# Kernel optimization log

Measured on AMD Instinct MI355X. Metric: run time of the kernel, lower is better.

Reference implementation:

```python
import jax, jax.numpy as jnp
import numpy as np

B, T, S, C = 4096, 128, 16, 128
NEG = -1e30  # finite stand-in for -inf to keep grads NaN-free


def setup_inputs() -> dict:
    key = jax.random.key(0)
    k1, k2 = jax.random.split(key)
    prediction = jax.random.normal(k1, (B, T, C), dtype=jnp.float32)  # treated as log-probs, as in the original
    lable = jax.random.normal(k2, (B, S, C), dtype=jnp.float32)       # one-hot-ish label scores
    return {"prediction": prediction, "lable": lable}


def _ctc_nll(logp, targets):
    """CTC negative log-likelihood, full-length inputs/targets.
    logp: (B, T, C) log-probabilities, blank=0. targets: (B, S) int.
    Returns nll: (B,)."""
    Bb, Tt, Cc = logp.shape
    Ss = targets.shape[1]
    L = 2 * Ss + 1  # extended label: blank-interleaved
    neg = jnp.float32(NEG)

    ext = jnp.zeros((Bb, L), dtype=targets.dtype).at[:, 1::2].set(targets)
    # skip transition l-2 -> l allowed iff ext[l] != ext[l-2] (auto-false on blanks)
    skip_ok = jnp.concatenate(
        [jnp.zeros((Bb, 2), dtype=bool), ext[:, 2:] != ext[:, :-2]], axis=1)

    # gather log-probs of extended labels for every time step: (B, T, L)
    logp_ext = jnp.take_along_axis(logp, ext[:, None, :], axis=2)

    alpha0 = (jnp.full((Bb, L), neg)
              .at[:, 0].set(logp_ext[:, 0, 0])
              .at[:, 1].set(logp_ext[:, 0, 1]))

    pad1 = jnp.full((Bb, 1), neg)
    pad2 = jnp.full((Bb, 2), neg)

    def step(alpha, lp_t):
        a1 = alpha
        a2 = jnp.concatenate([pad1, alpha[:, :-1]], axis=1)
        a3 = jnp.where(skip_ok, jnp.concatenate([pad2, alpha[:, :-2]], axis=1), neg)
        alpha_new = jnp.logaddexp(jnp.logaddexp(a1, a2), a3) + lp_t
        return alpha_new, None

    alpha_T, _ = jax.lax.scan(step, alpha0, jnp.swapaxes(logp_ext, 0, 1)[1:])
    nll = -jnp.logaddexp(alpha_T[:, -1], alpha_T[:, -2])
    return nll


def reference(prediction, lable):
    # synthesize_lable: per-(b,s) argmax over classes -> integer targets (B, S)
    targets = jnp.argmax(lable, axis=-1)
    nll = _ctc_nll(prediction, targets)
    # zero_infinity=True
    nll = jnp.where(jnp.isfinite(nll), nll, jnp.float32(0.0))
    # reduction='mean': divide each loss by its target length, then batch-mean
    Ss = lable.shape[1]
    return jnp.mean(nll / jnp.float32(Ss))
```

## Files before the change

kernel.cpp:

```cpp
#include <hip/hip_runtime.h>
#include <math.h>
#include <stdint.h>

#define B_ 4096
#define T_ 128
#define S_ 16
#define C_ 128
#define L_ 33
#define NSLOT 17
#define NELEM (T_ * NSLOT)
#define NEGV (-1e30f)
#define LOG2E 1.4426950408889634f
#define LN2 0.6931471805599453f
#define NEGB (NEGV * LOG2E)

__device__ __forceinline__ float hexp2(float x) { return __builtin_amdgcn_exp2f(x); }
__device__ __forceinline__ float hlog2(float x) { return __builtin_amdgcn_logf(x); }

__device__ __forceinline__ unsigned fkey(float v) {
    unsigned u = __float_as_uint(v);
    return (u & 0x80000000u) ? ~u : (u | 0x80000000u);
}

typedef const __attribute__((address_space(1))) unsigned int* gas_t;
typedef __attribute__((address_space(3))) unsigned int* las_t;

__global__ __launch_bounds__(256) void ctc_alpha_kernel(
        const float* __restrict__ pred,
        const float* __restrict__ lab,
        float* __restrict__ out_b) {
    const int wid  = threadIdx.x >> 6;
    const int lane = threadIdx.x & 63;
    const int b = blockIdx.x * 4 + wid;

    __shared__ int   cls_tab[4][NSLOT];
    __shared__ float lps[4][NELEM + 64];

    const int half = lane >> 5;
    const int li   = lane & 31;
    const float* lrow = lab + (size_t)b * S_ * C_ + (size_t)half * C_ + li;
    float vv[8][4];
    #pragma unroll
    for (int sp = 0; sp < 8; ++sp)
        #pragma unroll
        for (int k = 0; k < 4; ++k)
            vv[sp][k] = lrow[(size_t)sp * 2 * C_ + k * 32];

    if (lane == 0) cls_tab[wid][0] = 0;
    #pragma unroll
    for (int sp = 0; sp < 8; ++sp) {
        unsigned long long key = 0;
        #pragma unroll
        for (int k = 0; k < 4; ++k) {
            unsigned long long kk =
                ((unsigned long long)fkey(vv[sp][k]) << 32) | (unsigned)(~(li + 32 * k));
            if (kk > key) key = kk;
        }
        #pragma unroll
        for (int off = 16; off >= 1; off >>= 1) {
            unsigned long long ok = __shfl_xor(key, off, 64);
            if (ok > key) key = ok;
        }
        if (li == 0) cls_tab[wid][1 + sp * 2 + half] = (int)(~(unsigned)key) & 127;
    }
    asm volatile("s_waitcnt lgkmcnt(0)" ::: "memory");

    const float* pb = pred + (size_t)b * T_ * C_;
    float* mylds = lps[wid];
    #pragma unroll
    for (int i = 0; i < 34; ++i) {
        unsigned e = i * 64 + lane;
        unsigned t = e / NSLOT;
        unsigned s = e - t * NSLOT;
        int c = cls_tab[wid][s];
        const float* src = pb + (size_t)t * C_ + c;
        __builtin_amdgcn_global_load_lds((gas_t)src, (las_t)(mylds + i * 64), 4, 0, 0);
    }

    const int l = lane;
    int cidx = 0;
    bool skipv = false;
    if (l < L_ && (l & 1)) {
        cidx = 1 + ((l - 1) >> 1);
        if (l >= 3) skipv = (cls_tab[wid][cidx] != cls_tab[wid][cidx - 1]);
    }
    const bool has2 = (l >= 1);

    asm volatile("s_waitcnt vmcnt(17)" ::: "memory");

    float beta = (l <= 1) ? mylds[cidx] * LOG2E : NEGB;
    float lpA = mylds[1 * NSLOT + cidx];
    float lpB = mylds[2 * NSLOT + cidx];
    float lpC = mylds[3 * NSLOT + cidx];

    #pragma unroll 4
    for (int t = 1; t <= 60; ++t) {
        float lp = lpA; lpA = lpB; lpB = lpC;
        lpC = mylds[(t + 3) * NSLOT + cidx];
        float a2 = __shfl_up(beta, 1, 64);
        float a3 = __shfl_up(beta, 2, 64);
        a2 = has2  ? a2 : NEGB;
        a3 = skipv ? a3 : NEGB;
        float m = fmaxf(fmaxf(beta, a2), a3);
        float s = hexp2(beta - m) + hexp2(a2 - m) + hexp2(a3 - m);
        beta = fmaf(lp, LOG2E, m + hlog2(s));
    }

    asm volatile("s_waitcnt vmcnt(0)" ::: "memory");

    #pragma unroll 4
    for (int t = 61; t < T_; ++t) {
        float lp = lpA; lpA = lpB; lpB = lpC;
        lpC = mylds[(t + 3) * NSLOT + cidx];
        float a2 = __shfl_up(beta, 1, 64);
        float a3 = __shfl_up(beta, 2, 64);
        a2 = has2  ? a2 : NEGB;
        a3 = skipv ? a3 : NEGB;
        float m = fmaxf(fmaxf(beta, a2), a3);
        float s = hexp2(beta - m) + hexp2(a2 - m) + hexp2(a3 - m);
        beta = fmaf(lp, LOG2E, m + hlog2(s));
    }

    float b31 = __shfl(beta, L_ - 2, 64);
    float b32 = __shfl(beta, L_ - 1, 64);
    if (lane == 0) {
        float m = fmaxf(b31, b32);
        float lse2 = m + hlog2(hexp2(b31 - m) + hexp2(b32 - m));
        float nll = -lse2 * LN2;
        if (!isfinite(nll)) nll = 0.0f;
        out_b[b] = nll * (1.0f / (float)S_);
    }
}

__global__ __launch_bounds__(256) void reduce_mean_kernel(
        const float* __restrict__ in, float* __restrict__ out) {
    __shared__ float sm[256];
    const int tid = threadIdx.x;
    float v[16];
    #pragma unroll
    for (int i = 0; i < 16; ++i) v[i] = in[tid + i * 256];
    float s = 0.f;
    #pragma unroll
    for (int i = 0; i < 16; ++i) s += v[i];
    sm[tid] = s;
    __syncthreads();
    for (int w = 128; w >= 1; w >>= 1) {
        if (tid < w) sm[tid] += sm[tid + w];
        __syncthreads();
    }
    if (tid == 0) out[0] = sm[0] / (float)B_;
}

extern "C" void kernel_launch(void* const* d_in, const int* in_sizes, int n_in,
                              void* d_out, int out_size, void* d_ws, size_t ws_size,
                              hipStream_t stream) {
    const float* pred = (const float*)d_in[0];
    const float* lab  = (const float*)d_in[1];
    float* ws = (float*)d_ws;
    ctc_alpha_kernel<<<B_ / 4, 256, 0, stream>>>(pred, lab, ws);
    reduce_mean_kernel<<<1, 256, 0, stream>>>(ws, (float*)d_out);
}
```

Baseline: 63.10 us.

## Fuse mean reduction into CTC kernel via last-block atomic counter, one wave per block

Folds the separate batch-mean reduction kernel into the CTC alpha kernel: each block stores its per-sample loss and increments a global counter, and the last block to finish sums all losses. Blocks shrink from four waves to one wave per sample, label rows are loaded as float4, and sched_barriers split the gather-to-LDS loop. The aim is to remove the second kernel launch and its tail latency, at the cost of an extra memset launch and an atomic per block.

```diff
diff --git a/kernel.cpp b/kernel.cpp
--- a/kernel.cpp
+++ b/kernel.cpp
@@ -9,6 +9,7 @@
 #define L_ 33
 #define NSLOT 17
 #define NELEM (T_ * NSLOT)
+#define LDSF  (NELEM + 52)
 #define NEGV (-1e30f)
 #define LOG2E 1.4426950408889634f
 #define LN2 0.6931471805599453f
@@ -25,35 +26,36 @@
 typedef const __attribute__((address_space(1))) unsigned int* gas_t;
 typedef __attribute__((address_space(3))) unsigned int* las_t;
 
-__global__ __launch_bounds__(256) void ctc_alpha_kernel(
+__global__ __launch_bounds__(64) void ctc_fused_kernel(
         const float* __restrict__ pred,
         const float* __restrict__ lab,
-        float* __restrict__ out_b) {
-    const int wid  = threadIdx.x >> 6;
-    const int lane = threadIdx.x & 63;
-    const int b = blockIdx.x * 4 + wid;
+        float* __restrict__ out_b,
+        int* __restrict__ counter,
+        float* __restrict__ out) {
+    const int b = blockIdx.x;
+    const int lane = threadIdx.x;
 
-    __shared__ int   cls_tab[4][NSLOT];
-    __shared__ float lps[4][NELEM + 64];
+    __shared__ int   cls_tab[NSLOT];
+    __shared__ float lps[LDSF];
 
     const int half = lane >> 5;
     const int li   = lane & 31;
-    const float* lrow = lab + (size_t)b * S_ * C_ + (size_t)half * C_ + li;
-    float vv[8][4];
+    const float4* lrow4 =
+        (const float4*)(lab + (size_t)b * S_ * C_ + (size_t)half * C_);
+    float4 q[8];
     #pragma unroll
     for (int sp = 0; sp < 8; ++sp)
-        #pragma unroll
-        for (int k = 0; k < 4; ++k)
-            vv[sp][k] = lrow[(size_t)sp * 2 * C_ + k * 32];
+        q[sp] = lrow4[(size_t)sp * 2 * (C_ / 4) + li];
 
-    if (lane == 0) cls_tab[wid][0] = 0;
+    if (lane == 0) cls_tab[0] = 0;
     #pragma unroll
     for (int sp = 0; sp < 8; ++sp) {
+        float vals[4] = {q[sp].x, q[sp].y, q[sp].z, q[sp].w};
         unsigned long long key = 0;
         #pragma unroll
         for (int k = 0; k < 4; ++k) {
             unsigned long long kk =
-                ((unsigned long long)fkey(vv[sp][k]) << 32) | (unsigned)(~(li + 32 * k));
+                ((unsigned long long)fkey(vals[k]) << 32) | (unsigned)(~(li * 4 + k));
             if (kk > key) key = kk;
         }
         #pragma unroll
@@ -61,42 +63,50 @@
             unsigned long long ok = __shfl_xor(key, off, 64);
             if (ok > key) key = ok;
         }
-        if (li == 0) cls_tab[wid][1 + sp * 2 + half] = (int)(~(unsigned)key) & 127;
+        if (li == 0) cls_tab[1 + sp * 2 + half] = (int)(~(unsigned)key) & 127;
     }
     asm volatile("s_waitcnt lgkmcnt(0)" ::: "memory");
 
     const float* pb = pred + (size_t)b * T_ * C_;
-    float* mylds = lps[wid];
     #pragma unroll
-    for (int i = 0; i < 34; ++i) {
+    for (int i = 0; i < 17; ++i) {
         unsigned e = i * 64 + lane;
         unsigned t = e / NSLOT;
         unsigned s = e - t * NSLOT;
-        int c = cls_tab[wid][s];
-        const float* src = pb + (size_t)t * C_ + c;
-        __builtin_amdgcn_global_load_lds((gas_t)src, (las_t)(mylds + i * 64), 4, 0, 0);
+        const float* src = pb + (size_t)t * C_ + cls_tab[s];
+        __builtin_amdgcn_global_load_lds((gas_t)src, (las_t)(lps + i * 64), 4, 0, 0);
     }
+    __builtin_amdgcn_sched_barrier(0);
+    #pragma unroll
+    for (int i = 17; i < 34; ++i) {
+        unsigned e = i * 64 + lane;
+        unsigned t = e / NSLOT;
+        unsigned s = e - t * NSLOT;
+        const float* src = pb + (size_t)t * C_ + cls_tab[s];
+        __builtin_amdgcn_global_load_lds((gas_t)src, (las_t)(lps + i * 64), 4, 0, 0);
+    }
+    __builtin_amdgcn_sched_barrier(0);
 
     const int l = lane;
     int cidx = 0;
     bool skipv = false;
     if (l < L_ && (l & 1)) {
         cidx = 1 + ((l - 1) >> 1);
-        if (l >= 3) skipv = (cls_tab[wid][cidx] != cls_tab[wid][cidx - 1]);
+        if (l >= 3) skipv = (cls_tab[cidx] != cls_tab[cidx - 1]);
     }
     const bool has2 = (l >= 1);
 
     asm volatile("s_waitcnt vmcnt(17)" ::: "memory");
 
-    float beta = (l <= 1) ? mylds[cidx] * LOG2E : NEGB;
-    float lpA = mylds[1 * NSLOT + cidx];
-    float lpB = mylds[2 * NSLOT + cidx];
-    float lpC = mylds[3 * NSLOT + cidx];
+    float beta = (l <= 1) ? lps[cidx] * LOG2E : NEGB;
+    float lpA = lps[1 * NSLOT + cidx];
+    float lpB = lps[2 * NSLOT + cidx];
+    float lpC = lps[3 * NSLOT + cidx];
 
     #pragma unroll 4
     for (int t = 1; t <= 60; ++t) {
         float lp = lpA; lpA = lpB; lpB = lpC;
-        lpC = mylds[(t + 3) * NSLOT + cidx];
+        lpC = lps[(t + 3) * NSLOT + cidx];
         float a2 = __shfl_up(beta, 1, 64);
         float a3 = __shfl_up(beta, 2, 64);
         a2 = has2  ? a2 : NEGB;
@@ -111,7 +121,7 @@
     #pragma unroll 4
     for (int t = 61; t < T_; ++t) {
         float lp = lpA; lpA = lpB; lpB = lpC;
-        lpC = mylds[(t + 3) * NSLOT + cidx];
+        lpC = lps[(t + 3) * NSLOT + cidx];
         float a2 = __shfl_up(beta, 1, 64);
         float a3 = __shfl_up(beta, 2, 64);
         a2 = has2  ? a2 : NEGB;
@@ -123,32 +133,30 @@
 
     float b31 = __shfl(beta, L_ - 2, 64);
     float b32 = __shfl(beta, L_ - 1, 64);
-    if (lane == 0) {
-        float m = fmaxf(b31, b32);
-        float lse2 = m + hlog2(hexp2(b31 - m) + hexp2(b32 - m));
-        float nll = -lse2 * LN2;
-        if (!isfinite(nll)) nll = 0.0f;
-        out_b[b] = nll * (1.0f / (float)S_);
+    float m2 = fmaxf(b31, b32);
+    float nll = -(m2 + hlog2(hexp2(b31 - m2) + hexp2(b32 - m2))) * LN2;
+    if (!isfinite(nll)) nll = 0.0f;
+    float val = nll * (1.0f / (float)S_);
+    if (lane == 0)
+        __hip_atomic_store(&out_b[b], val, __ATOMIC_RELAXED, __HIP_MEMORY_SCOPE_AGENT);
+
+    int old = 0;
+    if (lane == 0)
+        old = __hip_atomic_fetch_add(counter, 1, __ATOMIC_ACQ_REL,
+                                     __HIP_MEMORY_SCOPE_AGENT);
+    old = __shfl(old, 0, 64);
+    if (old == B_ - 1) {
+        __threadfence();
+        float s = 0.f;
+        #pragma unroll
+        for (int i = 0; i < B_ / 64; ++i)
+            s += __hip_atomic_load(&out_b[lane + i * 64], __ATOMIC_RELAXED,
+                                   __HIP_MEMORY_SCOPE_AGENT);
+        #pragma unroll
+        for (int off = 1; off < 64; off <<= 1)
+            s += __shfl_xor(s, off, 64);
+        if (lane == 0) *out = s * (1.0f / (float)B_);
     }
-}
-
-__global__ __launch_bounds__(256) void reduce_mean_kernel(
-        const float* __restrict__ in, float* __restrict__ out) {
-    __shared__ float sm[256];
-    const int tid = threadIdx.x;
-    float v[16];
-    #pragma unroll
-    for (int i = 0; i < 16; ++i) v[i] = in[tid + i * 256];
-    float s = 0.f;
-    #pragma unroll
-    for (int i = 0; i < 16; ++i) s += v[i];
-    sm[tid] = s;
-    __syncthreads();
-    for (int w = 128; w >= 1; w >>= 1) {
-        if (tid < w) sm[tid] += sm[tid + w];
-        __syncthreads();
-    }
-    if (tid == 0) out[0] = sm[0] / (float)B_;
 }
 
 extern "C" void kernel_launch(void* const* d_in, const int* in_sizes, int n_in,
@@ -157,6 +165,7 @@
     const float* pred = (const float*)d_in[0];
     const float* lab  = (const float*)d_in[1];
     float* ws = (float*)d_ws;
-    ctc_alpha_kernel<<<B_ / 4, 256, 0, stream>>>(pred, lab, ws);
-    reduce_mean_kernel<<<1, 256, 0, stream>>>(ws, (float*)d_out);
+    int* counter = (int*)(ws + B_);
+    hipMemsetAsync(counter, 0, sizeof(int), stream);
+    ctc_fused_kernel<<<B_, 64, 0, stream>>>(pred, lab, ws, counter, (float*)d_out);
 }
```

Result: slower. 206.5 us (+227.3%).

## Process two batch rows per wave and overlap next row's loads with recurrence

Applied to the files above, without the earlier changes.

Each wave now handles two batch elements, with half as many blocks launched. The label argmax and log-prob gathers for the second element are issued while the alpha recurrence for the first is still running, so global-load latency is hidden behind compute. Label rows are also read as float4 vectors instead of strided scalar loads. The trade-off is half the number of waves in flight, which reduces latency hiding through occupancy, and a longer serial chain per wave.

```diff
diff --git a/kernel.cpp b/kernel.cpp
--- a/kernel.cpp
+++ b/kernel.cpp
@@ -9,6 +9,8 @@
 #define L_ 33
 #define NSLOT 17
 #define NELEM (T_ * NSLOT)
+#define LDSF  (NELEM + 64)
+#define NWAVE 2048
 #define NEGV (-1e30f)
 #define LOG2E 1.4426950408889634f
 #define LN2 0.6931471805599453f
@@ -25,111 +27,132 @@
 typedef const __attribute__((address_space(1))) unsigned int* gas_t;
 typedef __attribute__((address_space(3))) unsigned int* las_t;
 
-__global__ __launch_bounds__(256) void ctc_alpha_kernel(
+__global__ __launch_bounds__(256) void ctc_main_kernel(
         const float* __restrict__ pred,
         const float* __restrict__ lab,
         float* __restrict__ out_b) {
     const int wid  = threadIdx.x >> 6;
     const int lane = threadIdx.x & 63;
-    const int b = blockIdx.x * 4 + wid;
+    const int w = blockIdx.x * 4 + wid;
+    const int b0 = w, b1 = w + NWAVE;
 
     __shared__ int   cls_tab[4][NSLOT];
-    __shared__ float lps[4][NELEM + 64];
+    __shared__ float lps[4][LDSF];
+    int*   mytab = cls_tab[wid];
+    float* mylds = lps[wid];
 
     const int half = lane >> 5;
     const int li   = lane & 31;
-    const float* lrow = lab + (size_t)b * S_ * C_ + (size_t)half * C_ + li;
-    float vv[8][4];
-    #pragma unroll
-    for (int sp = 0; sp < 8; ++sp)
-        #pragma unroll
-        for (int k = 0; k < 4; ++k)
-            vv[sp][k] = lrow[(size_t)sp * 2 * C_ + k * 32];
-
-    if (lane == 0) cls_tab[wid][0] = 0;
-    #pragma unroll
-    for (int sp = 0; sp < 8; ++sp) {
-        unsigned long long key = 0;
-        #pragma unroll
-        for (int k = 0; k < 4; ++k) {
-            unsigned long long kk =
-                ((unsigned long long)fkey(vv[sp][k]) << 32) | (unsigned)(~(li + 32 * k));
-            if (kk > key) key = kk;
-        }
-        #pragma unroll
-        for (int off = 16; off >= 1; off >>= 1) {
-            unsigned long long ok = __shfl_xor(key, off, 64);
-            if (ok > key) key = ok;
-        }
-        if (li == 0) cls_tab[wid][1 + sp * 2 + half] = (int)(~(unsigned)key) & 127;
-    }
-    asm volatile("s_waitcnt lgkmcnt(0)" ::: "memory");
-
-    const float* pb = pred + (size_t)b * T_ * C_;
-    float* mylds = lps[wid];
-    #pragma unroll
-    for (int i = 0; i < 34; ++i) {
-        unsigned e = i * 64 + lane;
-        unsigned t = e / NSLOT;
-        unsigned s = e - t * NSLOT;
-        int c = cls_tab[wid][s];
-        const float* src = pb + (size_t)t * C_ + c;
-        __builtin_amdgcn_global_load_lds((gas_t)src, (las_t)(mylds + i * 64), 4, 0, 0);
-    }
 
     const int l = lane;
     int cidx = 0;
-    bool skipv = false;
-    if (l < L_ && (l & 1)) {
-        cidx = 1 + ((l - 1) >> 1);
-        if (l >= 3) skipv = (cls_tab[wid][cidx] != cls_tab[wid][cidx - 1]);
+    if (l < L_ && (l & 1)) cidx = 1 + ((l - 1) >> 1);
+    const bool has2 = (l >= 1);
+    const bool odd3 = (l < L_ && (l & 1) && l >= 3);
+
+    float4 q[8];
+    auto load_lab = [&](int b) {
+        const float4* lr = (const float4*)(lab + (size_t)b * S_ * C_ + (size_t)half * C_);
+        #pragma unroll
+        for (int sp = 0; sp < 8; ++sp)
+            q[sp] = lr[(size_t)sp * 2 * (C_ / 4) + li];
+    };
+    auto argmax_tab = [&]() {
+        if (lane == 0) mytab[0] = 0;
+        #pragma unroll
+        for (int sp = 0; sp < 8; ++sp) {
+            float vals[4] = {q[sp].x, q[sp].y, q[sp].z, q[sp].w};
+            unsigned long long key = 0;
+            #pragma unroll
+            for (int k = 0; k < 4; ++k) {
+                unsigned long long kk =
+                    ((unsigned long long)fkey(vals[k]) << 32) | (unsigned)(~(li * 4 + k));
+                if (kk > key) key = kk;
+            }
+            #pragma unroll
+            for (int off = 16; off >= 1; off >>= 1) {
+                unsigned long long ok = __shfl_xor(key, off, 64);
+                if (ok > key) key = ok;
+            }
+            if (li == 0) mytab[1 + sp * 2 + half] = (int)(~(unsigned)key) & 127;
+        }
+        asm volatile("s_waitcnt lgkmcnt(0)" ::: "memory");
+    };
+    auto stage = [&](const float* pb, int i0, int i1) {
+        for (int i = i0; i < i1; ++i) {
+            unsigned e = i * 64 + lane;
+            unsigned t = e / NSLOT;
+            unsigned s = e - t * NSLOT;
+            const float* src = pb + (size_t)t * C_ + mytab[s];
+            __builtin_amdgcn_global_load_lds((gas_t)src, (las_t)(mylds + i * 64), 4, 0, 0);
+        }
+        __builtin_amdgcn_sched_barrier(0);
+    };
+
+    float beta, lpA, lpB, lpC;
+    bool skipv;
+    auto ring_init = [&]() {
+        beta = (l <= 1) ? mylds[cidx] * LOG2E : NEGB;
+        lpA = mylds[1 * NSLOT + cidx];
+        lpB = mylds[2 * NSLOT + cidx];
+        lpC = mylds[3 * NSLOT + cidx];
+    };
+#define SEG(T0, T1)                                                         \
+    _Pragma("unroll 4")                                                     \
+    for (int t = (T0); t <= (T1); ++t) {                                    \
+        float lp = lpA; lpA = lpB; lpB = lpC;                               \
+        lpC = mylds[(t + 3) * NSLOT + cidx];                                \
+        float a2 = __shfl_up(beta, 1, 64);                                  \
+        float a3 = __shfl_up(beta, 2, 64);                                  \
+        a2 = has2  ? a2 : NEGB;                                             \
+        a3 = skipv ? a3 : NEGB;                                             \
+        float m = fmaxf(fmaxf(beta, a2), a3);                               \
+        float s = hexp2(beta - m) + hexp2(a2 - m) + hexp2(a3 - m);          \
+        beta = fmaf(lp, LOG2E, m + hlog2(s));                               \
     }
-    const bool has2 = (l >= 1);
+    auto finish = [&](int b) {
+        float b31 = __shfl(beta, L_ - 2, 64);
+        float b32 = __shfl(beta, L_ - 1, 64);
+        float m2 = fmaxf(b31, b32);
+        float nll = -(m2 + hlog2(hexp2(b31 - m2) + hexp2(b32 - m2))) * LN2;
+        if (!isfinite(nll)) nll = 0.0f;
+        if (lane == 0) out_b[b] = nll * (1.0f / (float)S_);
+    };
 
-    asm volatile("s_waitcnt vmcnt(17)" ::: "memory");
+    const float* pb0 = pred + (size_t)b0 * T_ * C_;
+    const float* pb1 = pred + (size_t)b1 * T_ * C_;
 
-    float beta = (l <= 1) ? mylds[cidx] * LOG2E : NEGB;
-    float lpA = mylds[1 * NSLOT + cidx];
-    float lpB = mylds[2 * NSLOT + cidx];
-    float lpC = mylds[3 * NSLOT + cidx];
+    load_lab(b0);
+    asm volatile("s_waitcnt vmcnt(0)" ::: "memory");
+    argmax_tab();
+    bool skip0 = odd3 && (mytab[cidx] != mytab[cidx - 1]);
+    stage(pb0, 0, 17);
+    stage(pb0, 17, 34);
+    load_lab(b1);
+    __builtin_amdgcn_sched_barrier(0);
 
-    #pragma unroll 4
-    for (int t = 1; t <= 60; ++t) {
-        float lp = lpA; lpA = lpB; lpB = lpC;
-        lpC = mylds[(t + 3) * NSLOT + cidx];
-        float a2 = __shfl_up(beta, 1, 64);
-        float a3 = __shfl_up(beta, 2, 64);
-        a2 = has2  ? a2 : NEGB;
-        a3 = skipv ? a3 : NEGB;
-        float m = fmaxf(fmaxf(beta, a2), a3);
-        float s = hexp2(beta - m) + hexp2(a2 - m) + hexp2(a3 - m);
-        beta = fmaf(lp, LOG2E, m + hlog2(s));
-    }
+    asm volatile("s_waitcnt vmcnt(25)" ::: "memory");
+    ring_init();
+    skipv = skip0;
+    SEG(1, 60)
 
     asm volatile("s_waitcnt vmcnt(0)" ::: "memory");
+    argmax_tab();
+    bool skip1 = odd3 && (mytab[cidx] != mytab[cidx - 1]);
+    stage(pb1, 0, 17);
+    SEG(61, 127)
+    finish(b0);
 
-    #pragma unroll 4
-    for (int t = 61; t < T_; ++t) {
-        float lp = lpA; lpA = lpB; lpB = lpC;
-        lpC = mylds[(t + 3) * NSLOT + cidx];
-        float a2 = __shfl_up(beta, 1, 64);
-        float a3 = __shfl_up(beta, 2, 64);
-        a2 = has2  ? a2 : NEGB;
-        a3 = skipv ? a3 : NEGB;
-        float m = fmaxf(fmaxf(beta, a2), a3);
-        float s = hexp2(beta - m) + hexp2(a2 - m) + hexp2(a3 - m);
-        beta = fmaf(lp, LOG2E, m + hlog2(s));
-    }
+    stage(pb1, 17, 34);
+    asm volatile("s_waitcnt vmcnt(17)" ::: "memory");
+    ring_init();
+    skipv = skip1;
+    SEG(1, 60)
 
-    float b31 = __shfl(beta, L_ - 2, 64);
-    float b32 = __shfl(beta, L_ - 1, 64);
-    if (lane == 0) {
-        float m = fmaxf(b31, b32);
-        float lse2 = m + hlog2(hexp2(b31 - m) + hexp2(b32 - m));
-        float nll = -lse2 * LN2;
-        if (!isfinite(nll)) nll = 0.0f;
-        out_b[b] = nll * (1.0f / (float)S_);
-    }
+    asm volatile("s_waitcnt vmcnt(0)" ::: "memory");
+    SEG(61, 127)
+    finish(b1);
+#undef SEG
 }
 
 __global__ __launch_bounds__(256) void reduce_mean_kernel(
@@ -157,6 +180,6 @@
     const float* pred = (const float*)d_in[0];
     const float* lab  = (const float*)d_in[1];
     float* ws = (float*)d_ws;
-    ctc_alpha_kernel<<<B_ / 4, 256, 0, stream>>>(pred, lab, ws);
+    ctc_main_kernel<<<NWAVE / 4, 256, 0, stream>>>(pred, lab, ws);
     reduce_mean_kernel<<<1, 256, 0, stream>>>(ws, (float*)d_out);
 }
```

Result: slower. 65.81 us (+4.3%).
